# Kernel tuning notes

Hardware: AMD Instinct MI355X
Metric: run time of the kernel (lower is better)

## Reference

```python
import jax, jax.numpy as jnp
import numpy as np

B, S, D, DQK, DV = 4, 2048, 1024, 128, 256
EPS = 1e-8


def setup_inputs() -> dict:
    key = jax.random.key(0)
    ks = jax.random.split(key, 11)
    s = lambda fan_in: 1.0 / np.sqrt(fan_in)
    return {
        "X": jax.random.normal(ks[0], (B, S, D), dtype=jnp.float32),
        "Wq": jax.random.uniform(ks[1], (D, DQK), minval=-s(D), maxval=s(D), dtype=jnp.float32),
        "bq": jax.random.uniform(ks[2], (DQK,), minval=-s(D), maxval=s(D), dtype=jnp.float32),
        "Wk": jax.random.uniform(ks[3], (D, DQK), minval=-s(D), maxval=s(D), dtype=jnp.float32),
        "bk": jax.random.uniform(ks[4], (DQK,), minval=-s(D), maxval=s(D), dtype=jnp.float32),
        "Wv": jax.random.uniform(ks[5], (D, DV), minval=-s(D), maxval=s(D), dtype=jnp.float32),
        "bv": jax.random.uniform(ks[6], (DV,), minval=-s(D), maxval=s(D), dtype=jnp.float32),
        "Wg": jax.random.uniform(ks[7], (D, DV), minval=-s(D), maxval=s(D), dtype=jnp.float32),
        "bg": jax.random.uniform(ks[8], (DV,), minval=-s(D), maxval=s(D), dtype=jnp.float32),
        "Wp": jax.random.uniform(ks[9], (DV, D), minval=-s(DV), maxval=s(DV), dtype=jnp.float32),
        "bp": jax.random.uniform(ks[10], (D,), minval=-s(DV), maxval=s(DV), dtype=jnp.float32),
    }


def _shepards(Q, K, V, p=2, eps=EPS):
    # Euclidean cdist via ||q||^2 + ||k||^2 - 2 q.k  (then sqrt)
    q2 = jnp.sum(Q * Q, axis=-1, keepdims=True)          # [B,Sq,1]
    k2 = jnp.sum(K * K, axis=-1, keepdims=True)          # [B,Sk,1]
    d2 = q2 + jnp.swapaxes(k2, -1, -2) - 2.0 * jnp.einsum("bqd,bkd->bqk", Q, K)
    Dm = jnp.sqrt(jnp.maximum(d2, 0.0))                  # [B,Sq,Sk]
    W = jnp.power(jnp.maximum(Dm, eps), -float(p))
    A = W / jnp.sum(W, axis=2, keepdims=True)
    return jnp.einsum("bqk,bkv->bqv", A, V)


def reference(X, Wq, bq, Wk, bk, Wv, bv, Wg, bg, Wp, bp):
    N = X  # norm is Identity
    Q = N @ Wq + bq
    K = N @ Wk + bk
    V = N @ Wv + bv
    A = _shepards(Q, K, V)
    G = N @ Wg + bg
    return X + (A * G) @ Wp + bp
```

## Files before the change

### kernel.cpp

```cpp
#include <hip/hip_runtime.h>
#include <stdint.h>

#define SLEN 2048
#define NROWS 8192

typedef __attribute__((ext_vector_type(4))) float f32x4;
typedef __attribute__((ext_vector_type(8))) short bf16x8;
typedef __attribute__((ext_vector_type(2))) unsigned int u32x2;

__device__ __forceinline__ short f2bf(float f) {
  uint32_t u = __builtin_bit_cast(uint32_t, f);
  u += 0x7FFFu + ((u >> 16) & 1u);
  return (short)(u >> 16);
}
__device__ __forceinline__ float bf2f(short s) {
  uint32_t u = ((uint32_t)(uint16_t)s) << 16;
  return __builtin_bit_cast(float, u);
}
__device__ __forceinline__ f32x4 mfma16(bf16x8 a, bf16x8 b, f32x4 c) {
  return __builtin_amdgcn_mfma_f32_16x16x32_bf16(a, b, c, 0, 0, 0);
}
__device__ __forceinline__ void gld_lds16(const void* g, void* l) {
  __builtin_amdgcn_global_load_lds(
      (const __attribute__((address_space(1))) void*)g,
      (__attribute__((address_space(3))) void*)l, 16, 0, 0);
}

__global__ __launch_bounds__(256) void k_prep(
    const float* __restrict__ X,
    const float* __restrict__ Wq, const float* __restrict__ bq,
    const float* __restrict__ Wk, const float* __restrict__ bk,
    const float* __restrict__ Wv, const float* __restrict__ bv,
    const float* __restrict__ Wg, const float* __restrict__ bg,
    const float* __restrict__ Wp,
    short* __restrict__ Xb, short* __restrict__ WcatT,
    short* __restrict__ WpT, float* __restrict__ bcat) {
  __shared__ short tl[64][72];
  int blk = blockIdx.x, tid = threadIdx.x;
  if (blk < 4096) {
    size_t e = ((size_t)blk * 256 + tid) * 8;
    f32x4 a = *(const f32x4*)&X[e];
    f32x4 b = *(const f32x4*)&X[e + 4];
    bf16x8 o;
    o[0] = f2bf(a[0]); o[1] = f2bf(a[1]); o[2] = f2bf(a[2]); o[3] = f2bf(a[3]);
    o[4] = f2bf(b[0]); o[5] = f2bf(b[1]); o[6] = f2bf(b[2]); o[7] = f2bf(b[3]);
    *(bf16x8*)&Xb[e] = o;
  } else if (blk < 4352) {
    int t = blk - 4096;
    const float* src; short* dst; int C, rowoff, dstC, r0, c0;
    if (t < 32)       { src = Wq; C = 128;  rowoff = 0;   dst = WcatT; dstC = 1024; r0 = (t >> 1) * 64;  c0 = (t & 1) * 64; }
    else if (t < 64)  { t -= 32;  src = Wk; C = 128;  rowoff = 128; dst = WcatT; dstC = 1024; r0 = (t >> 1) * 64;  c0 = (t & 1) * 64; }
    else if (t < 128) { t -= 64;  src = Wv; C = 256;  rowoff = 256; dst = WcatT; dstC = 1024; r0 = (t >> 2) * 64;  c0 = (t & 3) * 64; }
    else if (t < 192) { t -= 128; src = Wg; C = 256;  rowoff = 512; dst = WcatT; dstC = 1024; r0 = (t >> 2) * 64;  c0 = (t & 3) * 64; }
    else              { t -= 192; src = Wp; C = 1024; rowoff = 0;   dst = WpT;   dstC = 256;  r0 = (t >> 4) * 64;  c0 = (t & 15) * 64; }
    int lr = tid >> 4, lcc = tid & 15;
#pragma unroll
    for (int rr = 0; rr < 4; ++rr) {
      f32x4 v = *(const f32x4*)&src[(size_t)(r0 + lr * 4 + rr) * C + c0 + lcc * 4];
#pragma unroll
      for (int j = 0; j < 4; ++j) tl[lcc * 4 + j][lr * 4 + rr] = f2bf(v[j]);
    }
    __syncthreads();
    int orow = tid >> 2, og = (tid & 3) * 16;
    bf16x8 o1, o2;
#pragma unroll
    for (int j = 0; j < 8; ++j) { o1[j] = tl[orow][og + j]; o2[j] = tl[orow][og + 8 + j]; }
    size_t dbase = (size_t)(rowoff + c0 + orow) * dstC + r0 + og;
    *(bf16x8*)&dst[dbase] = o1;
    *(bf16x8*)&dst[dbase + 8] = o2;
  } else {
    int c = tid;
    if (c < 768) {
      float v;
      if (c < 128)      v = bq[c];
      else if (c < 256) v = bk[c - 128];
      else if (c < 512) v = bv[c - 256];
      else              v = bg[c - 512];
      bcat[c] = v;
    }
  }
}

__global__ __launch_bounds__(256) void k_gemm1(
    const short* __restrict__ Xb, const short* __restrict__ WcatT,
    const float* __restrict__ bcat, short* __restrict__ O,
    float* __restrict__ q2a, float* __restrict__ k2a) {
  __shared__ short At[128 * 32];
  __shared__ short Bt[128 * 32];
  __shared__ float nlds[128][2];
  const int tid = threadIdx.x;
  const int w = tid >> 6, l = tid & 63, lg = l >> 4, lc = l & 15;
  const int m0 = blockIdx.x * 128, n0 = blockIdx.y * 128;
  const int sr0 = w * 32 + (l >> 2);
  const int scc = (l & 3) * 8;
  const int wm = (w >> 1) * 64, wn = (w & 1) * 64;

  f32x4 acc[4][4] = {};
  const short* Ab = Xb + (size_t)m0 * 1024;
  const short* Bb = WcatT + (size_t)n0 * 1024;

  for (int kb = 0; kb < 1024; kb += 32) {
    gld_lds16(Ab + (size_t)sr0 * 1024 + kb + scc, &At[(w * 32) * 32]);
    gld_lds16(Ab + (size_t)(sr0 + 16) * 1024 + kb + scc, &At[(w * 32 + 16) * 32]);
    gld_lds16(Bb + (size_t)sr0 * 1024 + kb + scc, &Bt[(w * 32) * 32]);
    gld_lds16(Bb + (size_t)(sr0 + 16) * 1024 + kb + scc, &Bt[(w * 32 + 16) * 32]);
    __syncthreads();
    bf16x8 af[4], bf[4];
#pragma unroll
    for (int mi = 0; mi < 4; ++mi)
      af[mi] = *(const bf16x8*)&At[(wm + mi * 16 + lc) * 32 + lg * 8];
#pragma unroll
    for (int ni = 0; ni < 4; ++ni)
      bf[ni] = *(const bf16x8*)&Bt[(wn + ni * 16 + lc) * 32 + lg * 8];
#pragma unroll
    for (int mi = 0; mi < 4; ++mi)
#pragma unroll
      for (int ni = 0; ni < 4; ++ni)
        acc[mi][ni] = mfma16(af[mi], bf[ni], acc[mi][ni]);
    __syncthreads();
  }
  float sq[4][4] = {};
#pragma unroll
  for (int mi = 0; mi < 4; ++mi) {
    int gr = m0 + wm + mi * 16 + lg * 4;
#pragma unroll
    for (int ni = 0; ni < 4; ++ni) {
      int gc = n0 + wn + ni * 16 + lc;
      float bias = bcat[gc];
#pragma unroll
      for (int r = 0; r < 4; ++r) {
        short sv = f2bf(acc[mi][ni][r] + bias);
        O[(size_t)(gr + r) * 768 + gc] = sv;
        float v = bf2f(sv);
        sq[mi][r] += v * v;
      }
    }
  }
  if (blockIdx.y < 2) {
#pragma unroll
    for (int mi = 0; mi < 4; ++mi)
#pragma unroll
      for (int r = 0; r < 4; ++r) {
        float v = sq[mi][r];
        v += __shfl_xor(v, 1, 64); v += __shfl_xor(v, 2, 64);
        v += __shfl_xor(v, 4, 64); v += __shfl_xor(v, 8, 64);
        sq[mi][r] = v;
      }
    if (lc == 0) {
#pragma unroll
      for (int mi = 0; mi < 4; ++mi)
#pragma unroll
        for (int r = 0; r < 4; ++r)
          nlds[wm + mi * 16 + lg * 4 + r][w & 1] = sq[mi][r];
    }
    __syncthreads();
    if (tid < 128) {
      float t = nlds[tid][0] + nlds[tid][1];
      (blockIdx.y == 0 ? q2a : k2a)[m0 + tid] = t;
    }
  }
}

__global__ __launch_bounds__(256) void k_vt(
    const short* __restrict__ O, short* __restrict__ Vt) {
  __shared__ short tile[64][33];
  int blk = blockIdx.x, tid = threadIdx.x;
  int b = blk >> 8, rem = blk & 255;
  int s0 = (rem >> 3) * 64, dv0 = (rem & 7) * 32;
  int r = tid >> 2, cg = (tid & 3) * 8;
  bf16x8 v = *(const bf16x8*)&O[(size_t)(b * SLEN + s0 + r) * 768 + 256 + dv0 + cg];
#pragma unroll
  for (int j = 0; j < 8; ++j) tile[r][cg + j] = v[j];
  __syncthreads();
  int dr = tid >> 3, sg = (tid & 7) * 8;
  bf16x8 ov;
#pragma unroll
  for (int j = 0; j < 8; ++j) ov[j] = tile[sg + j][dr];
  *(bf16x8*)&Vt[(size_t)(b * 256 + dv0 + dr) * SLEN + s0 + sg] = ov;
}

__global__ __launch_bounds__(256) void k_attn(
    const short* __restrict__ O, const short* __restrict__ Vt,
    const float* __restrict__ q2a, const float* __restrict__ k2a,
    short* __restrict__ nump, float* __restrict__ denp) {
  __shared__ short Wt[32 * 256];
  __shared__ float dls[4][32];
  const int tid = threadIdx.x;
  const int w = tid >> 6, l = tid & 63, lg = l >> 4, lc = l & 15;
  const int blk = ((blockIdx.x & 7) << 7) | (blockIdx.x >> 3);
  const int ks = blk & 3;
  const int qt = (blk >> 2) & 63;
  const int b = blk >> 8;
  const int grow0 = b * SLEN + qt * 32;

  bf16x8 qf[2][4];
#pragma unroll
  for (int mi = 0; mi < 2; ++mi)
#pragma unroll
    for (int kf = 0; kf < 4; ++kf)
      qf[mi][kf] = *(const bf16x8*)&O[(size_t)(grow0 + mi * 16 + lc) * 768 + kf * 32 + lg * 8];

  float q2s[2];
  q2s[0] = q2a[grow0 + lc];
  q2s[1] = q2a[grow0 + 16 + lc];

  f32x4 acc[2][4] = {};
  float den0 = 0.f, den1 = 0.f;

  for (int it = 0; it < 2; ++it) {
    const int kt = ks * 512 + it * 256;
    const int krow = b * SLEN + kt + w * 64;
    f32x4 s[2][4] = {};
#pragma unroll
    for (int nk = 0; nk < 4; ++nk) {
#pragma unroll
      for (int kf = 0; kf < 4; ++kf) {
        bf16x8 kv = *(const bf16x8*)&O[(size_t)(krow + nk * 16 + lc) * 768 + 128 + kf * 32 + lg * 8];
        s[0][nk] = mfma16(kv, qf[0][kf], s[0][nk]);
        s[1][nk] = mfma16(kv, qf[1][kf], s[1][nk]);
      }
    }
#pragma unroll
    for (int nk = 0; nk < 4; ++nk) {
      f32x4 k2v = *(const f32x4*)&k2a[krow + nk * 16 + lg * 4];
      float wv[2][4];
#pragma unroll
      for (int mi = 0; mi < 2; ++mi)
#pragma unroll
        for (int r = 0; r < 4; ++r) {
          float d2 = q2s[mi] + k2v[r] - 2.0f * s[mi][nk][r];
          d2 = fmaxf(d2, 1e-16f);
          wv[mi][r] = __builtin_amdgcn_rcpf(d2);
        }
      den0 += wv[0][0] + wv[0][1] + wv[0][2] + wv[0][3];
      den1 += wv[1][0] + wv[1][1] + wv[1][2] + wv[1][3];
      int col = w * 64 + nk * 16 + lg * 4;
#pragma unroll
      for (int mi = 0; mi < 2; ++mi) {
        u32x2 pk;
        pk[0] = (uint32_t)(uint16_t)f2bf(wv[mi][0]) | ((uint32_t)(uint16_t)f2bf(wv[mi][1]) << 16);
        pk[1] = (uint32_t)(uint16_t)f2bf(wv[mi][2]) | ((uint32_t)(uint16_t)f2bf(wv[mi][3]) << 16);
        int q = mi * 16 + lc;
        int byte = q * 512 + col * 2;
        byte ^= (q & 7) << 4;
        *(u32x2*)((char*)Wt + byte) = pk;
      }
    }
    __syncthreads();
#pragma unroll
    for (int kf2 = 0; kf2 < 8; ++kf2) {
      bf16x8 af0, af1;
      {
        int rr = lc;
        int byte = rr * 512 + kf2 * 64 + lg * 16; byte ^= (rr & 7) << 4;
        af0 = *(const bf16x8*)((const char*)Wt + byte);
      }
      {
        int rr = 16 + lc;
        int byte = rr * 512 + kf2 * 64 + lg * 16; byte ^= (rr & 7) << 4;
        af1 = *(const bf16x8*)((const char*)Wt + byte);
      }
#pragma unroll
      for (int nv = 0; nv < 4; ++nv) {
        bf16x8 bv = *(const bf16x8*)&Vt[(size_t)(b * 256 + w * 64 + nv * 16 + lc) * SLEN + kt + kf2 * 32 + lg * 8];
        acc[0][nv] = mfma16(af0, bv, acc[0][nv]);
        acc[1][nv] = mfma16(af1, bv, acc[1][nv]);
      }
    }
    __syncthreads();
  }
  den0 += __shfl_xor(den0, 16, 64); den0 += __shfl_xor(den0, 32, 64);
  den1 += __shfl_xor(den1, 16, 64); den1 += __shfl_xor(den1, 32, 64);
  if (l < 16) { dls[w][lc] = den0; dls[w][16 + lc] = den1; }
  __syncthreads();
  const size_t pbase = (size_t)blk * 32 * 256;
#pragma unroll
  for (int mi = 0; mi < 2; ++mi)
#pragma unroll
    for (int nv = 0; nv < 4; ++nv) {
      int dv = w * 64 + nv * 16 + lc;
#pragma unroll
      for (int r = 0; r < 4; ++r) {
        int rit = mi * 16 + lg * 4 + r;
        nump[pbase + (size_t)rit * 256 + dv] = f2bf(acc[mi][nv][r]);
      }
    }
  if (tid < 32)
    denp[blk * 32 + tid] = dls[0][tid] + dls[1][tid] + dls[2][tid] + dls[3][tid];
}

__global__ __launch_bounds__(256) void k_red(
    const short* __restrict__ nump, const float* __restrict__ denp,
    const short* __restrict__ O, short* __restrict__ AG) {
  int flat = blockIdx.x * 256 + threadIdx.x;
  int idx8 = flat * 8;
  int row = idx8 >> 8;
  int dv0 = idx8 & 255;
  int b = row >> 11, srow = row & 2047;
  int qt = srow >> 5, rit = srow & 31;
  int blkbase = (b * 64 + qt) << 2;
  float num[8] = {};
  float den = 0.f;
#pragma unroll
  for (int ksi = 0; ksi < 4; ++ksi) {
    const size_t base = ((size_t)(blkbase + ksi) * 32 + rit) * 256 + dv0;
    bf16x8 v = *(const bf16x8*)&nump[base];
#pragma unroll
    for (int j = 0; j < 8; ++j) num[j] += bf2f(v[j]);
    den += denp[(blkbase + ksi) * 32 + rit];
  }
  float rden = 1.f / den;
  bf16x8 gv = *(const bf16x8*)&O[(size_t)row * 768 + 512 + dv0];
  bf16x8 o;
#pragma unroll
  for (int j = 0; j < 8; ++j) o[j] = f2bf(num[j] * rden * bf2f(gv[j]));
  *(bf16x8*)&AG[idx8] = o;
}

__global__ __launch_bounds__(256) void k_gemm3(
    const short* __restrict__ AG, const short* __restrict__ WpT,
    const float* __restrict__ X, const float* __restrict__ bp,
    float* __restrict__ Y) {
  __shared__ short At[128 * 32];
  __shared__ short Bt[128 * 32];
  const int tid = threadIdx.x;
  const int w = tid >> 6, l = tid & 63, lg = l >> 4, lc = l & 15;
  const int m0 = blockIdx.x * 128, n0 = blockIdx.y * 128;
  const int sr0 = w * 32 + (l >> 2);
  const int scc = (l & 3) * 8;
  const int wm = (w >> 1) * 64, wn = (w & 1) * 64;

  f32x4 acc[4][4] = {};
  const short* Ab = AG + (size_t)m0 * 256;
  const short* Bb = WpT + (size_t)n0 * 256;

  for (int kb = 0; kb < 256; kb += 32) {
    gld_lds16(Ab + (size_t)sr0 * 256 + kb + scc, &At[(w * 32) * 32]);
    gld_lds16(Ab + (size_t)(sr0 + 16) * 256 + kb + scc, &At[(w * 32 + 16) * 32]);
    gld_lds16(Bb + (size_t)sr0 * 256 + kb + scc, &Bt[(w * 32) * 32]);
    gld_lds16(Bb + (size_t)(sr0 + 16) * 256 + kb + scc, &Bt[(w * 32 + 16) * 32]);
    __syncthreads();
    bf16x8 af[4], bf[4];
#pragma unroll
    for (int mi = 0; mi < 4; ++mi)
      af[mi] = *(const bf16x8*)&At[(wm + mi * 16 + lc) * 32 + lg * 8];
#pragma unroll
    for (int ni = 0; ni < 4; ++ni)
      bf[ni] = *(const bf16x8*)&Bt[(wn + ni * 16 + lc) * 32 + lg * 8];
#pragma unroll
    for (int mi = 0; mi < 4; ++mi)
#pragma unroll
      for (int ni = 0; ni < 4; ++ni)
        acc[mi][ni] = mfma16(af[mi], bf[ni], acc[mi][ni]);
    __syncthreads();
  }
#pragma unroll
  for (int mi = 0; mi < 4; ++mi) {
    int gr = m0 + wm + mi * 16 + lg * 4;
#pragma unroll
    for (int ni = 0; ni < 4; ++ni) {
      int gc = n0 + wn + ni * 16 + lc;
      float bias = bp[gc];
#pragma unroll
      for (int r = 0; r < 4; ++r) {
        size_t idx = (size_t)(gr + r) * 1024 + gc;
        Y[idx] = acc[mi][ni][r] + X[idx] + bias;
      }
    }
  }
}

extern "C" void kernel_launch(void* const* d_in, const int* in_sizes, int n_in,
                              void* d_out, int out_size, void* d_ws, size_t ws_size,
                              hipStream_t stream) {
  const float* X  = (const float*)d_in[0];
  const float* Wq = (const float*)d_in[1];
  const float* bq = (const float*)d_in[2];
  const float* Wk = (const float*)d_in[3];
  const float* bk = (const float*)d_in[4];
  const float* Wv = (const float*)d_in[5];
  const float* bv = (const float*)d_in[6];
  const float* Wg = (const float*)d_in[7];
  const float* bg = (const float*)d_in[8];
  const float* Wp = (const float*)d_in[9];
  const float* bp = (const float*)d_in[10];

  char* ws = (char*)d_ws;
  short* Xb    = (short*)(ws + 0);
  short* WcatT = (short*)(ws + 16777216);
  short* WpT   = (short*)(ws + 18350080);
  float* bcat  = (float*)(ws + 18874368);
  short* O     = (short*)(ws + 18878464);
  short* Vt    = (short*)(ws + 31461376);
  float* q2a   = (float*)(ws + 35655680);
  float* k2a   = (float*)(ws + 35688448);
  short* AG    = (short*)(ws + 35721216);
  short* nump  = (short*)(ws + 0);
  float* denp  = (float*)(ws + 16777216);
  float* Y = (float*)d_out;

  hipLaunchKernelGGL(k_prep, dim3(4353), dim3(256), 0, stream,
                     X, Wq, bq, Wk, bk, Wv, bv, Wg, bg, Wp, Xb, WcatT, WpT, bcat);
  hipLaunchKernelGGL(k_gemm1, dim3(64, 6), dim3(256), 0, stream, Xb, WcatT, bcat, O, q2a, k2a);
  hipLaunchKernelGGL(k_vt, dim3(1024), dim3(256), 0, stream, O, Vt);
  hipLaunchKernelGGL(k_attn, dim3(1024), dim3(256), 0, stream, O, Vt, q2a, k2a, nump, denp);
  hipLaunchKernelGGL(k_red, dim3(1024), dim3(256), 0, stream, nump, denp, O, AG);
  hipLaunchKernelGGL(k_gemm3, dim3(64, 8), dim3(256), 0, stream, AG, WpT, X, bp, Y);
}
```

Measured before the change: 214.3 us.

## Keep Shepard weights in registers via permuted V layout, drop LDS round-trip

k_vt now writes V transposed in a permuted key order that matches the MFMA accumulator output layout. k_attn can then feed the bf16-converted weights straight from registers as the A operand of the second MFMA, with no swizzled LDS write and no barriers inside the loop. Work is re-split so that each wave pair covers half the key range and half of DV, and the two partial accumulators are summed through LDS at the end. This adds a larger shared buffer and more accumulator registers (launch bounds 256,2), which may limit occupancy.

Result: slower. 226.8 us (+5.9%).

```diff
diff --git a/kernel.cpp b/kernel.cpp
--- a/kernel.cpp
+++ b/kernel.cpp
@@ -7,6 +7,7 @@
 typedef __attribute__((ext_vector_type(4))) float f32x4;
 typedef __attribute__((ext_vector_type(8))) short bf16x8;
 typedef __attribute__((ext_vector_type(2))) unsigned int u32x2;
+typedef __attribute__((ext_vector_type(4))) unsigned int u32x4;
 
 __device__ __forceinline__ short f2bf(float f) {
   uint32_t u = __builtin_bit_cast(uint32_t, f);
@@ -162,7 +163,7 @@
 }
 
 __global__ __launch_bounds__(256) void k_vt(
-    const short* __restrict__ O, short* __restrict__ Vt) {
+    const short* __restrict__ O, short* __restrict__ Vtp) {
   __shared__ short tile[64][33];
   int blk = blockIdx.x, tid = threadIdx.x;
   int b = blk >> 8, rem = blk & 255;
@@ -176,22 +177,30 @@
   bf16x8 ov;
 #pragma unroll
   for (int j = 0; j < 8; ++j) ov[j] = tile[sg + j][dr];
-  *(bf16x8*)&Vt[(size_t)(b * 256 + dv0 + dr) * SLEN + s0 + sg] = ov;
-}
-
-__global__ __launch_bounds__(256) void k_attn(
-    const short* __restrict__ O, const short* __restrict__ Vt,
+  int ka = s0 + sg;
+  int c5 = ka >> 5, hi = (ka >> 4) & 1, lgq = (ka >> 2) & 3;
+  size_t base = (size_t)(b * 256 + dv0 + dr) * SLEN + c5 * 32 + lgq * 8 + hi * 4;
+  u32x4 od = __builtin_bit_cast(u32x4, ov);
+  u32x2 p0; p0[0] = od[0]; p0[1] = od[1];
+  u32x2 p1; p1[0] = od[2]; p1[1] = od[3];
+  *(u32x2*)&Vtp[base] = p0;
+  *(u32x2*)&Vtp[base + 8] = p1;
+}
+
+__global__ __launch_bounds__(256, 2) void k_attn(
+    const short* __restrict__ O, const short* __restrict__ Vtp,
     const float* __restrict__ q2a, const float* __restrict__ k2a,
     short* __restrict__ nump, float* __restrict__ denp) {
-  __shared__ short Wt[32 * 256];
-  __shared__ float dls[4][32];
+  __shared__ float reg4[4][16][64][4];
+  __shared__ float dls[2][32];
   const int tid = threadIdx.x;
   const int w = tid >> 6, l = tid & 63, lg = l >> 4, lc = l & 15;
+  const int h = w >> 1, dh = w & 1;
   const int blk = ((blockIdx.x & 7) << 7) | (blockIdx.x >> 3);
-  const int ks = blk & 3;
-  const int qt = (blk >> 2) & 63;
-  const int b = blk >> 8;
+  const int ks = blk & 3, qt = (blk >> 2) & 63, b = blk >> 8;
   const int grow0 = b * SLEN + qt * 32;
+  const int kloc0 = ks * 512 + h * 256;
+  const int krow0 = b * SLEN + kloc0;
 
   bf16x8 qf[2][4];
 #pragma unroll
@@ -204,89 +213,80 @@
   q2s[0] = q2a[grow0 + lc];
   q2s[1] = q2a[grow0 + 16 + lc];
 
-  f32x4 acc[2][4] = {};
+  f32x4 acc[2][8] = {};
   float den0 = 0.f, den1 = 0.f;
-
-  for (int it = 0; it < 2; ++it) {
-    const int kt = ks * 512 + it * 256;
-    const int krow = b * SLEN + kt + w * 64;
-    f32x4 s[2][4] = {};
-#pragma unroll
-    for (int nk = 0; nk < 4; ++nk) {
+  const short* vbase = Vtp + (size_t)(b * 256 + dh * 128 + lc) * SLEN;
+
+#pragma unroll 2
+  for (int c = 0; c < 8; ++c) {
+    const int kr = krow0 + c * 32;
+    f32x4 s[2][2] = {};
+#pragma unroll
+    for (int e = 0; e < 2; ++e)
 #pragma unroll
       for (int kf = 0; kf < 4; ++kf) {
-        bf16x8 kv = *(const bf16x8*)&O[(size_t)(krow + nk * 16 + lc) * 768 + 128 + kf * 32 + lg * 8];
-        s[0][nk] = mfma16(kv, qf[0][kf], s[0][nk]);
-        s[1][nk] = mfma16(kv, qf[1][kf], s[1][nk]);
+        bf16x8 kv = *(const bf16x8*)&O[(size_t)(kr + e * 16 + lc) * 768 + 128 + kf * 32 + lg * 8];
+        s[0][e] = mfma16(kv, qf[0][kf], s[0][e]);
+        s[1][e] = mfma16(kv, qf[1][kf], s[1][e]);
       }
-    }
-#pragma unroll
-    for (int nk = 0; nk < 4; ++nk) {
-      f32x4 k2v = *(const f32x4*)&k2a[krow + nk * 16 + lg * 4];
-      float wv[2][4];
+    float wv[2][2][4];
+#pragma unroll
+    for (int e = 0; e < 2; ++e) {
+      f32x4 k2v = *(const f32x4*)&k2a[kr + e * 16 + lg * 4];
 #pragma unroll
       for (int mi = 0; mi < 2; ++mi)
 #pragma unroll
         for (int r = 0; r < 4; ++r) {
-          float d2 = q2s[mi] + k2v[r] - 2.0f * s[mi][nk][r];
-          d2 = fmaxf(d2, 1e-16f);
-          wv[mi][r] = __builtin_amdgcn_rcpf(d2);
+          float d2 = q2s[mi] + k2v[r] - 2.0f * s[mi][e][r];
+          wv[mi][e][r] = __builtin_amdgcn_rcpf(fmaxf(d2, 1e-16f));
         }
-      den0 += wv[0][0] + wv[0][1] + wv[0][2] + wv[0][3];
-      den1 += wv[1][0] + wv[1][1] + wv[1][2] + wv[1][3];
-      int col = w * 64 + nk * 16 + lg * 4;
-#pragma unroll
-      for (int mi = 0; mi < 2; ++mi) {
-        u32x2 pk;
-        pk[0] = (uint32_t)(uint16_t)f2bf(wv[mi][0]) | ((uint32_t)(uint16_t)f2bf(wv[mi][1]) << 16);
-        pk[1] = (uint32_t)(uint16_t)f2bf(wv[mi][2]) | ((uint32_t)(uint16_t)f2bf(wv[mi][3]) << 16);
-        int q = mi * 16 + lc;
-        int byte = q * 512 + col * 2;
-        byte ^= (q & 7) << 4;
-        *(u32x2*)((char*)Wt + byte) = pk;
+    }
+#pragma unroll
+    for (int r = 0; r < 4; ++r) {
+      den0 += wv[0][0][r] + wv[0][1][r];
+      den1 += wv[1][0][r] + wv[1][1][r];
+    }
+    bf16x8 pa[2];
+#pragma unroll
+    for (int mi = 0; mi < 2; ++mi) {
+#pragma unroll
+      for (int r = 0; r < 4; ++r) {
+        pa[mi][r] = f2bf(wv[mi][0][r]);
+        pa[mi][4 + r] = f2bf(wv[mi][1][r]);
       }
     }
-    __syncthreads();
-#pragma unroll
-    for (int kf2 = 0; kf2 < 8; ++kf2) {
-      bf16x8 af0, af1;
-      {
-        int rr = lc;
-        int byte = rr * 512 + kf2 * 64 + lg * 16; byte ^= (rr & 7) << 4;
-        af0 = *(const bf16x8*)((const char*)Wt + byte);
-      }
-      {
-        int rr = 16 + lc;
-        int byte = rr * 512 + kf2 * 64 + lg * 16; byte ^= (rr & 7) << 4;
-        af1 = *(const bf16x8*)((const char*)Wt + byte);
-      }
-#pragma unroll
-      for (int nv = 0; nv < 4; ++nv) {
-        bf16x8 bv = *(const bf16x8*)&Vt[(size_t)(b * 256 + w * 64 + nv * 16 + lc) * SLEN + kt + kf2 * 32 + lg * 8];
-        acc[0][nv] = mfma16(af0, bv, acc[0][nv]);
-        acc[1][nv] = mfma16(af1, bv, acc[1][nv]);
-      }
-    }
-    __syncthreads();
+    const int voff = kloc0 + c * 32 + lg * 8;
+#pragma unroll
+    for (int nv = 0; nv < 8; ++nv) {
+      bf16x8 bv = *(const bf16x8*)&vbase[(size_t)nv * 16 * SLEN + voff];
+      acc[0][nv] = mfma16(pa[0], bv, acc[0][nv]);
+      acc[1][nv] = mfma16(pa[1], bv, acc[1][nv]);
+    }
   }
   den0 += __shfl_xor(den0, 16, 64); den0 += __shfl_xor(den0, 32, 64);
   den1 += __shfl_xor(den1, 16, 64); den1 += __shfl_xor(den1, 32, 64);
-  if (l < 16) { dls[w][lc] = den0; dls[w][16 + lc] = den1; }
+  if (dh == 0 && l < 16) { dls[h][l] = den0; dls[h][16 + l] = den1; }
+#pragma unroll
+  for (int mi = 0; mi < 2; ++mi)
+#pragma unroll
+    for (int nv = 0; nv < 8; ++nv)
+      *(f32x4*)&reg4[w][mi * 8 + nv][l][0] = acc[mi][nv];
   __syncthreads();
   const size_t pbase = (size_t)blk * 32 * 256;
-#pragma unroll
-  for (int mi = 0; mi < 2; ++mi)
-#pragma unroll
-    for (int nv = 0; nv < 4; ++nv) {
-      int dv = w * 64 + nv * 16 + lc;
-#pragma unroll
-      for (int r = 0; r < 4; ++r) {
-        int rit = mi * 16 + lg * 4 + r;
-        nump[pbase + (size_t)rit * 256 + dv] = f2bf(acc[mi][nv][r]);
-      }
-    }
-  if (tid < 32)
-    denp[blk * 32 + tid] = dls[0][tid] + dls[1][tid] + dls[2][tid] + dls[3][tid];
+  const int dh_o = w >> 1;
+#pragma unroll
+  for (int i = 0; i < 8; ++i) {
+    int lcb = (w & 1) * 8 + i;
+    int mi = lcb >> 3, nv = lcb & 7;
+    f32x4 a = *(const f32x4*)&reg4[dh_o][lcb][l][0];
+    f32x4 c2 = *(const f32x4*)&reg4[dh_o + 2][lcb][l][0];
+    int dv = dh_o * 128 + nv * 16 + lc;
+    int rb = mi * 16 + lg * 4;
+#pragma unroll
+    for (int r = 0; r < 4; ++r)
+      nump[pbase + (size_t)(rb + r) * 256 + dv] = f2bf(a[r] + c2[r]);
+  }
+  if (tid < 32) denp[blk * 32 + tid] = dls[0][tid] + dls[1][tid];
 }
 
 __global__ __launch_bounds__(256) void k_red(
@@ -391,7 +391,7 @@
   short* WpT   = (short*)(ws + 18350080);
   float* bcat  = (float*)(ws + 18874368);
   short* O     = (short*)(ws + 18878464);
-  short* Vt    = (short*)(ws + 31461376);
+  short* Vtp   = (short*)(ws + 31461376);
   float* q2a   = (float*)(ws + 35655680);
   float* k2a   = (float*)(ws + 35688448);
   short* AG    = (short*)(ws + 35721216);
@@ -402,8 +402,8 @@
   hipLaunchKernelGGL(k_prep, dim3(4353), dim3(256), 0, stream,
                      X, Wq, bq, Wk, bk, Wv, bv, Wg, bg, Wp, Xb, WcatT, WpT, bcat);
   hipLaunchKernelGGL(k_gemm1, dim3(64, 6), dim3(256), 0, stream, Xb, WcatT, bcat, O, q2a, k2a);
-  hipLaunchKernelGGL(k_vt, dim3(1024), dim3(256), 0, stream, O, Vt);
-  hipLaunchKernelGGL(k_attn, dim3(1024), dim3(256), 0, stream, O, Vt, q2a, k2a, nump, denp);
+  hipLaunchKernelGGL(k_vt, dim3(1024), dim3(256), 0, stream, O, Vtp);
+  hipLaunchKernelGGL(k_attn, dim3(1024), dim3(256), 0, stream, O, Vtp, q2a, k2a, nump, denp);
   hipLaunchKernelGGL(k_red, dim3(1024), dim3(256), 0, stream, nump, denp, O, AG);
   hipLaunchKernelGGL(k_gemm3, dim3(64, 8), dim3(256), 0, stream, AG, WpT, X, bp, Y);
 }
```
